# Optimization experiments

Measured on AMD Instinct MI355X. Metric: run time of the kernel, lower is better.

Reference implementation:

```python
import jax, jax.numpy as jnp
import numpy as np

B, NV, L, NKG = 8, 100, 128, 923
NT = NV + 1 + NKG  # 1024 total nodes
DV, DK, DH, H, NLAYERS, VOCAB = 2048, 300, 1024, 8, 3, 50265
DHD = DH // H


def _ln(x, g, b, eps=1e-5):
    m = x.mean(-1, keepdims=True)
    v = x.var(-1, keepdims=True)
    return (x - m) / jnp.sqrt(v + eps) * g + b


def _gat_layer(x, mask, W, bb, a_src, a_dst, ln_g, ln_b):
    # x: [B,N,D], mask: [B,N,N] bool
    Bn, N, D = x.shape
    h = (x @ W + bb).reshape(Bn, N, H, DHD)
    s = jnp.einsum('bnhd,hd->bnh', h, a_src)  # source term
    t = jnp.einsum('bnhd,hd->bnh', h, a_dst)  # target term
    e = jax.nn.leaky_relu(s[:, :, None, :] + t[:, None, :, :], 0.2)  # [B,N,N,H]
    e = jnp.where(mask[..., None], e, -1e9)
    a = jax.nn.softmax(e, axis=2)  # over neighbors j
    out = jnp.einsum('bijh,bjhd->bihd', a, h).reshape(Bn, N, D)
    return _ln(x + out, ln_g, ln_b)


def setup_inputs() -> dict:
    key = jax.random.key(0)
    ks = jax.random.split(key, 24)
    s = 0.02
    inp = {
        'visual_features': jax.random.normal(ks[0], (B, NV, DV), jnp.float32),
        'question_input_ids': jax.random.randint(ks[1], (B, L), 0, VOCAB, jnp.int64) if False else jax.random.randint(ks[1], (B, L), 0, VOCAB).astype(jnp.int32),
        'question_attention_mask': jnp.ones((B, L), jnp.int32),
        'graph_node_features': jax.random.normal(ks[2], (B, NKG, DK), jnp.float32),
        'graph_adj': jax.random.randint(ks[3], (B, NT, NT), 0, 2).astype(jnp.int32),
        'graph_node_types': jax.random.randint(ks[4], (B, NT), 0, 3).astype(jnp.int32),
        # params
        'vis_W': jax.random.normal(ks[5], (DV, DH), jnp.float32) * s,
        'vis_b': jnp.zeros((DH,), jnp.float32),
        'vis_ln_g': jnp.ones((DH,), jnp.float32),
        'vis_ln_b': jnp.zeros((DH,), jnp.float32),
        'tok_emb': jax.random.normal(ks[6], (VOCAB, DH), jnp.float32) * s,
        'q_W': jax.random.normal(ks[7], (DH, DH), jnp.float32) * s,
        'q_b': jnp.zeros((DH,), jnp.float32),
        'q_ln_g': jnp.ones((DH,), jnp.float32),
        'q_ln_b': jnp.zeros((DH,), jnp.float32),
        'kg_W': jax.random.normal(ks[8], (DK, DH), jnp.float32) * s,
        'kg_b': jnp.zeros((DH,), jnp.float32),
        'kg_ln_g': jnp.ones((DH,), jnp.float32),
        'kg_ln_b': jnp.zeros((DH,), jnp.float32),
        'type_emb': jax.random.normal(ks[9], (3, DH), jnp.float32) * s,
        'gat_W': jax.random.normal(ks[10], (NLAYERS, DH, DH), jnp.float32) * s,
        'gat_b': jnp.zeros((NLAYERS, DH), jnp.float32),
        'a_src': jax.random.normal(ks[11], (NLAYERS, H, DHD), jnp.float32) * s,
        'a_dst': jax.random.normal(ks[12], (NLAYERS, H, DHD), jnp.float32) * s,
        'gat_ln_g': jnp.ones((NLAYERS, DH), jnp.float32),
        'gat_ln_b': jnp.zeros((NLAYERS, DH), jnp.float32),
        'readout_W': jax.random.normal(ks[13], (DH, 1), jnp.float32) * s,
        'readout_b': jnp.zeros((1,), jnp.float32),
        'cs_W1': jax.random.normal(ks[14], (DH, DH), jnp.float32) * s,
        'cs_b1': jnp.zeros((DH,), jnp.float32),
        'cs_W2': jax.random.normal(ks[15], (DH, 1), jnp.float32) * s,
        'cs_b2': jnp.zeros((1,), jnp.float32),
    }
    return inp


def reference(visual_features, question_input_ids, question_attention_mask,
              graph_node_features, graph_adj, graph_node_types,
              vis_W, vis_b, vis_ln_g, vis_ln_b,
              tok_emb, q_W, q_b, q_ln_g, q_ln_b,
              kg_W, kg_b, kg_ln_g, kg_ln_b,
              type_emb, gat_W, gat_b, a_src, a_dst, gat_ln_g, gat_ln_b,
              readout_W, readout_b, cs_W1, cs_b1, cs_W2, cs_b2):
    # 1. visual projection
    vis = _ln(visual_features @ vis_W + vis_b, vis_ln_g, vis_ln_b)  # [B,NV,DH]
    # 2. text encoder (embedding + masked mean-pool + proj + LN)
    te = tok_emb[question_input_ids]  # [B,L,DH]
    m = question_attention_mask.astype(te.dtype)[..., None]
    pooled = (te * m).sum(1) / jnp.maximum(m.sum(1), 1.0)
    q = _ln(pooled @ q_W + q_b, q_ln_g, q_ln_b)[:, None, :]  # [B,1,DH]
    # 3. KG projection
    kg = _ln(graph_node_features @ kg_W + kg_b, kg_ln_g, kg_ln_b)
    # 4-5. concat + node-type embeddings
    x = jnp.concatenate([vis, q, kg], axis=1) + type_emb[graph_node_types]
    # 6. dense GAT stack
    mask = graph_adj > 0
    for l in range(NLAYERS):
        x = _gat_layer(x, mask, gat_W[l], gat_b[l], a_src[l], a_dst[l],
                       gat_ln_g[l], gat_ln_b[l])
    # 7. attention-pooled readout
    w = jax.nn.softmax((x @ readout_W + readout_b).squeeze(-1), axis=-1)
    g = (x * w[..., None]).sum(1)  # [B,DH]
    # 8. candidate scorer
    logits = jax.nn.gelu(g @ cs_W1 + cs_b1) @ cs_W2 + cs_b2  # [B,1]
    return logits
```

## Files before the change

### kernel.cpp

```cpp
#include <hip/hip_runtime.h>
#include <math.h>

#define NB 8
#define NV 100
#define LQ 128
#define NKG 923
#define NT 1024
#define DV 2048
#define DK 300
#define DH 1024
#define NH 8
#define DHD 128
#define NLAYERS 3

typedef __attribute__((ext_vector_type(8))) short short8;
typedef __attribute__((ext_vector_type(4))) float f32x4;

__device__ __forceinline__ short f2bf(float f) {
    unsigned u = __float_as_uint(f);
    u += 0x7fff + ((u >> 16) & 1);
    return (short)(u >> 16);
}
__device__ __forceinline__ float bf2f(short s) {
    unsigned u = ((unsigned)(unsigned short)s) << 16;
    return __uint_as_float(u);
}
__device__ __forceinline__ unsigned pack2(float a, float b) {
    return (unsigned)(unsigned short)f2bf(a) | ((unsigned)(unsigned short)f2bf(b) << 16);
}

#if __has_builtin(__builtin_amdgcn_global_load_lds)
#define HAVE_GLL 1
__device__ __forceinline__ void gll16(const void* g, void* l) {
    __builtin_amdgcn_global_load_lds(
        (const __attribute__((address_space(1))) void*)g,
        (__attribute__((address_space(3))) void*)l, 16, 0, 0);
}
#else
#define HAVE_GLL 0
#endif

__device__ __forceinline__ float block_reduce_sum(float v, float* red) {
    int tid = threadIdx.x;
    red[tid] = v; __syncthreads();
    for (int s = 128; s > 0; s >>= 1) {
        if (tid < s) red[tid] += red[tid + s];
        __syncthreads();
    }
    float r = red[0]; __syncthreads();
    return r;
}
__device__ __forceinline__ float block_reduce_max(float v, float* red) {
    int tid = threadIdx.x;
    red[tid] = v; __syncthreads();
    for (int s = 128; s > 0; s >>= 1) {
        if (tid < s) red[tid] = fmaxf(red[tid], red[tid + s]);
        __syncthreads();
    }
    float r = red[0]; __syncthreads();
    return r;
}

__global__ __launch_bounds__(256) void bitmask_kernel(
    const int* __restrict__ adj, unsigned* __restrict__ mb)
{
    int bi = blockIdx.x;
    int tid = threadIdx.x;
#pragma unroll
    for (int p = 0; p < 4; ++p) {
        int j = p * 256 + tid;
        unsigned long long bal = __ballot(adj[(size_t)bi * NT + j] > 0);
        if ((tid & 63) == 0) {
            int w = (p * 256 + (tid & 0xC0)) >> 5;
            mb[(size_t)bi * 32 + w]     = (unsigned)bal;
            mb[(size_t)bi * 32 + w + 1] = (unsigned)(bal >> 32);
        }
    }
}

__global__ __launch_bounds__(256) void transpose_cast(
    const float* __restrict__ in, short* __restrict__ out,
    int K, int N, int Kp)
{
    __shared__ float ls[64][65];
    int n0 = blockIdx.x * 64, k0 = blockIdx.y * 64;
    int tid = threadIdx.x;
    int j4 = (tid & 15) * 4;
#pragma unroll
    for (int s = 0; s < 4; ++s) {
        int i = (tid >> 4) + s * 16;
        int k = k0 + i;
        float4 v = make_float4(0.f, 0.f, 0.f, 0.f);
        if (k < K) v = *(const float4*)(in + (size_t)k * N + n0 + j4);
        ls[i][j4 + 0] = v.x; ls[i][j4 + 1] = v.y;
        ls[i][j4 + 2] = v.z; ls[i][j4 + 3] = v.w;
    }
    __syncthreads();
#pragma unroll
    for (int s = 0; s < 4; ++s) {
        int a = (tid >> 4) + s * 16;
        int b = (tid & 15) * 4;
        uint2 pk;
        pk.x = pack2(ls[b + 0][a], ls[b + 1][a]);
        pk.y = pack2(ls[b + 2][a], ls[b + 3][a]);
        *(uint2*)(out + (size_t)(n0 + a) * Kp + k0 + b) = pk;
    }
}

__global__ __launch_bounds__(256) void gemm_bias_mfma(
    const float* __restrict__ A, const short* __restrict__ Wt,
    const float* __restrict__ bias, float* __restrict__ C,
    int M, int N, int K, int Kp, int ldA)
{
    __shared__ short At[128][32];
    __shared__ short Bt[128][32];
    int tid = threadIdx.x;
    int row0 = blockIdx.y * 128, col0 = blockIdx.x * 128;
    int lane = tid & 63, wave = tid >> 6;
    int quad = lane >> 4, lq = lane & 15;
    int wm = (wave >> 1) * 64, wn = (wave & 1) * 64;
    f32x4 acc[4][4];
#pragma unroll
    for (int i = 0; i < 4; ++i)
#pragma unroll
        for (int j = 0; j < 4; ++j) {
            f32x4 z = {0.f, 0.f, 0.f, 0.f};
            acc[i][j] = z;
        }
    int ar = tid >> 2;
    int ac = (tid & 3) * 8;
    for (int k0 = 0; k0 < Kp; k0 += 32) {
        bool fullk = (k0 + 32 <= K);
#pragma unroll
        for (int s = 0; s < 2; ++s) {
            int r = ar + s * 64;
            int grow = row0 + r;
            short8 pk;
            if (grow < M && fullk) {
                const float* src = A + (size_t)grow * ldA + k0 + ac;
                float4 v0 = *(const float4*)(src);
                float4 v1 = *(const float4*)(src + 4);
                pk[0] = f2bf(v0.x); pk[1] = f2bf(v0.y);
                pk[2] = f2bf(v0.z); pk[3] = f2bf(v0.w);
                pk[4] = f2bf(v1.x); pk[5] = f2bf(v1.y);
                pk[6] = f2bf(v1.z); pk[7] = f2bf(v1.w);
            } else {
#pragma unroll
                for (int e = 0; e < 8; ++e) {
                    int k = k0 + ac + e;
                    pk[e] = (grow < M && k < K)
                          ? f2bf(A[(size_t)grow * ldA + k]) : (short)0;
                }
            }
            *(short8*)&At[r][ac] = pk;
        }
#pragma unroll
        for (int s = 0; s < 2; ++s) {
            int n = ar + s * 64;
            short8 w = *(const short8*)(Wt + (size_t)(col0 + n) * Kp + k0 + ac);
            *(short8*)&Bt[n][ac] = w;
        }
        __syncthreads();
        short8 af[4], bfr[4];
#pragma unroll
        for (int i = 0; i < 4; ++i)
            af[i] = *(short8*)&At[wm + i * 16 + lq][quad * 8];
#pragma unroll
        for (int j = 0; j < 4; ++j)
            bfr[j] = *(short8*)&Bt[wn + j * 16 + lq][quad * 8];
#pragma unroll
        for (int i = 0; i < 4; ++i)
#pragma unroll
            for (int j = 0; j < 4; ++j)
                acc[i][j] = __builtin_amdgcn_mfma_f32_16x16x32_bf16(
                    af[i], bfr[j], acc[i][j], 0, 0, 0);
        __syncthreads();
    }
#pragma unroll
    for (int j = 0; j < 4; ++j) {
        int n = col0 + wn + j * 16 + lq;
        float bv = bias[n];
#pragma unroll
        for (int i = 0; i < 4; ++i) {
#pragma unroll
            for (int r = 0; r < 4; ++r) {
                int m = row0 + wm + i * 16 + quad * 4 + r;
                if (m < M) C[(size_t)m * N + n] = acc[i][j][r] + bv;
            }
        }
    }
}

__global__ __launch_bounds__(256) void gemm_st_mfma(
    const short* __restrict__ Ab, const short* __restrict__ Wt,
    const float* __restrict__ bias,
    const float* __restrict__ asrc, const float* __restrict__ adst,
    short* __restrict__ ht,
    float* __restrict__ sbuf, float* __restrict__ tbuf)
{
    __shared__ __align__(16) short smem[17408];
    short (*At)[32]  = (short(*)[32])smem;
    short (*Bt)[32]  = (short(*)[32])(smem + 4096);
    short (*ct)[136] = (short(*)[136])smem;
    __shared__ float sred[2][128], tred[2][128];
    __shared__ float asl[128], adl[128];
    int tid = threadIdx.x;
    int h = blockIdx.x;
    int row0 = blockIdx.y * 128, col0 = h * 128;
    int b = row0 >> 10, i0 = row0 & 1023;
    int lane = tid & 63, wave = tid >> 6;
    int quad = lane >> 4, lq = lane & 15;
    int wm = (wave >> 1) * 64, wn = (wave & 1) * 64;
    if (tid < 128) asl[tid] = asrc[h * DHD + tid];
    else adl[tid - 128] = adst[h * DHD + tid - 128];
    f32x4 acc[4][4];
#pragma unroll
    for (int i = 0; i < 4; ++i)
#pragma unroll
        for (int j = 0; j < 4; ++j) {
            f32x4 z = {0.f, 0.f, 0.f, 0.f};
            acc[i][j] = z;
        }

    const short* gA0 = Ab + (size_t)(row0 + wave * 16 + (lane >> 2)) * DH + (lane & 3) * 8;
    const short* gA1 = gA0 + (size_t)64 * DH;
    const short* gB0 = Wt + (size_t)(col0 + wave * 16 + (lane >> 2)) * DH + (lane & 3) * 8;
    const short* gB1 = gB0 + (size_t)64 * DH;
#if HAVE_GLL
    char* lA0 = (char*)At + wave * 1024; char* lA1 = lA0 + 4096;
    char* lB0 = (char*)Bt + wave * 1024; char* lB1 = lB0 + 4096;
#endif
    for (int k0 = 0; k0 < DH; k0 += 32) {
#if HAVE_GLL
        gll16(gA0 + k0, lA0); gll16(gA1 + k0, lA1);
        gll16(gB0 + k0, lB0); gll16(gB1 + k0, lB1);
#else
        {
            short8 va0 = *(const short8*)(gA0 + k0);
            short8 va1 = *(const short8*)(gA1 + k0);
            short8 vb0 = *(const short8*)(gB0 + k0);
            short8 vb1 = *(const short8*)(gB1 + k0);
            *(short8*)((char*)At + wave * 1024 + lane * 16) = va0;
            *(short8*)((char*)At + 4096 + wave * 1024 + lane * 16) = va1;
            *(short8*)((char*)Bt + wave * 1024 + lane * 16) = vb0;
            *(short8*)((char*)Bt + 4096 + wave * 1024 + lane * 16) = vb1;
        }
#endif
        __syncthreads();
        short8 af[4], bfr[4];
#pragma unroll
        for (int i = 0; i < 4; ++i)
            af[i] = *(short8*)&At[wm + i * 16 + lq][quad * 8];
#pragma unroll
        for (int j = 0; j < 4; ++j)
            bfr[j] = *(short8*)&Bt[wn + j * 16 + lq][quad * 8];
#pragma unroll
        for (int i = 0; i < 4; ++i)
#pragma unroll
            for (int j = 0; j < 4; ++j)
                acc[i][j] = __builtin_amdgcn_mfma_f32_16x16x32_bf16(
                    af[i], bfr[j], acc[i][j], 0, 0, 0);
        __syncthreads();
    }
#pragma unroll
    for (int j = 0; j < 4; ++j) {
        int d = wn + j * 16 + lq;
        float bv = bias[col0 + d];
#pragma unroll
        for (int i2 = 0; i2 < 4; ++i2) {
            int m = wm + i2 * 16 + quad * 4;
            uint2 pk;
            pk.x = pack2(acc[i2][j][0] + bv, acc[i2][j][1] + bv);
            pk.y = pack2(acc[i2][j][2] + bv, acc[i2][j][3] + bv);
            *(uint2*)&ct[d][m] = pk;
        }
    }
    __syncthreads();
    {
        int d = tid >> 1, half = tid & 1;
        short* dst = ht + ((size_t)(b * NH + h) * DHD + d) * NT + i0 + half * 64;
        const short* src = &ct[d][half * 64];
#pragma unroll
        for (int q = 0; q < 8; ++q)
            *(short8*)(dst + q * 8) = *(const short8*)(src + q * 8);
    }
    {
        int i = tid >> 1, half = tid & 1;
        float sa = 0.f, ta = 0.f;
#pragma unroll 16
        for (int dd = 0; dd < 64; ++dd) {
            int d = half * 64 + dd;
            float hv = bf2f(ct[d][i]);
            sa += hv * asl[d];
            ta += hv * adl[d];
        }
        sred[half][i] = sa; tred[half][i] = ta;
    }
    __syncthreads();
    if (tid < 128) {
        size_t idx = (size_t)(b * NH + h) * NT + i0 + tid;
        sbuf[idx] = sred[0][tid] + sred[1][tid];
        tbuf[idx] = tred[0][tid] + tred[1][tid];
    }
}

__global__ __launch_bounds__(256) void ln_scatter(
    const float* __restrict__ src, float* __restrict__ x,
    const float* __restrict__ g, const float* __restrict__ bta,
    int rows, int npb, int node_off)
{
    __shared__ float red[256];
    int r = blockIdx.x;
    if (r >= rows) return;
    int tid = threadIdx.x;
    int b = r / npb, n = r % npb;
    float4 v = *(const float4*)(src + (size_t)r * DH + tid * 4);
    float s = v.x + v.y + v.z + v.w;
    float sq = v.x * v.x + v.y * v.y + v.z * v.z + v.w * v.w;
    float tot = block_reduce_sum(s, red);
    float totsq = block_reduce_sum(sq, red);
    float mean = tot * (1.0f / DH);
    float var = totsq * (1.0f / DH) - mean * mean;
    float rstd = 1.0f / sqrtf(var + 1e-5f);
    float4 gv = *(const float4*)(g + tid * 4);
    float4 bv = *(const float4*)(bta + tid * 4);
    float4 o;
    o.x = (v.x - mean) * rstd * gv.x + bv.x;
    o.y = (v.y - mean) * rstd * gv.y + bv.y;
    o.z = (v.z - mean) * rstd * gv.z + bv.z;
    o.w = (v.w - mean) * rstd * gv.w + bv.w;
    *(float4*)(x + ((size_t)(b * NT + node_off + n)) * DH + tid * 4) = o;
}

__global__ __launch_bounds__(256) void ln_residual(
    float* __restrict__ x, const float* __restrict__ o,
    const float* __restrict__ g, const float* __restrict__ bta,
    short* __restrict__ xb,
    const float* __restrict__ rW, const float* __restrict__ rb,
    float* __restrict__ scores)
{
    __shared__ float red[256];
    int r = blockIdx.x;
    int tid = threadIdx.x;
    float* xr = x + (size_t)r * DH;
    float4 xv = *(float4*)(xr + tid * 4);
    float4 ov = *(const float4*)(o + (size_t)r * DH + tid * 4);
    float v0 = xv.x + ov.x, v1 = xv.y + ov.y, v2 = xv.z + ov.z, v3 = xv.w + ov.w;
    float s = v0 + v1 + v2 + v3;
    float sq = v0 * v0 + v1 * v1 + v2 * v2 + v3 * v3;
    float tot = block_reduce_sum(s, red);
    float totsq = block_reduce_sum(sq, red);
    float mean = tot * (1.0f / DH);
    float var = totsq * (1.0f / DH) - mean * mean;
    float rstd = 1.0f / sqrtf(var + 1e-5f);
    float4 gv = *(const float4*)(g + tid * 4);
    float4 bv = *(const float4*)(bta + tid * 4);
    float4 out;
    out.x = (v0 - mean) * rstd * gv.x + bv.x;
    out.y = (v1 - mean) * rstd * gv.y + bv.y;
    out.z = (v2 - mean) * rstd * gv.z + bv.z;
    out.w = (v3 - mean) * rstd * gv.w + bv.w;
    *(float4*)(xr + tid * 4) = out;
    uint2 pk;
    pk.x = pack2(out.x, out.y);
    pk.y = pack2(out.z, out.w);
    *(uint2*)(xb + (size_t)r * DH + tid * 4) = pk;
    if (scores) {
        float4 wv = *(const float4*)(rW + tid * 4);
        float p = out.x * wv.x + out.y * wv.y + out.z * wv.z + out.w * wv.w;
        float totp = block_reduce_sum(p, red);
        if (tid == 0) scores[r] = totp + rb[0];
    }
}

__global__ __launch_bounds__(256) void pool_kernel(
    const float* __restrict__ tok_emb, const int* __restrict__ ids,
    const int* __restrict__ amask, float* __restrict__ pooled)
{
    int b = blockIdx.x;
    int tid = threadIdx.x;
    float a0 = 0, a1 = 0, a2 = 0, a3 = 0;
    float denom = 0;
    for (int l = 0; l < LQ; ++l) {
        int id = ids[b * LQ + l];
        float m = (float)amask[b * LQ + l];
        denom += m;
        float4 e = *(const float4*)(tok_emb + (size_t)id * DH + tid * 4);
        a0 += m * e.x; a1 += m * e.y; a2 += m * e.z; a3 += m * e.w;
    }
    float inv = 1.0f / fmaxf(denom, 1.0f);
    float4 o = make_float4(a0 * inv, a1 * inv, a2 * inv, a3 * inv);
    *(float4*)(pooled + b * DH + tid * 4) = o;
}

__global__ __launch_bounds__(256) void type_add(
    float* __restrict__ x, const int* __restrict__ types,
    const float* __restrict__ type_emb, short* __restrict__ xb)
{
    int r = blockIdx.x;
    int tid = threadIdx.x;
    int ty = types[r];
    float4 xv = *(float4*)(x + (size_t)r * DH + tid * 4);
    float4 tv = *(const float4*)(type_emb + (size_t)ty * DH + tid * 4);
    xv.x += tv.x; xv.y += tv.y; xv.z += tv.z; xv.w += tv.w;
    *(float4*)(x + (size_t)r * DH + tid * 4) = xv;
    uint2 pk;
    pk.x = pack2(xv.x, xv.y);
    pk.y = pack2(xv.z, xv.w);
    *(uint2*)(xb + (size_t)r * DH + tid * 4) = pk;
}

__global__ __launch_bounds__(256) void agg_mfma(
    const short* __restrict__ ht, const unsigned* __restrict__ mb,
    const float* __restrict__ s, const float* __restrict__ t,
    float* __restrict__ obuf)
{
    __shared__ short vt[128][72];
    __shared__ short at[64][72];
    __shared__ unsigned mrow[64][32];
    __shared__ float sv[64], alpha_s[64], lfin[64];
    int i0 = blockIdx.x * 64;
    int h = blockIdx.y, b = blockIdx.z;
    int tid = threadIdx.x;
    int lane = tid & 63, wave = tid >> 6;
    int quad = lane >> 4, lq = lane & 15;
    int wi = (wave >> 1) * 32;
    int wd = (wave & 1) * 64;
    if (tid < 64) sv[tid] = s[(size_t)(b * NH + h) * NT + i0 + tid];
#pragma unroll
    for (int s2 = 0; s2 < 2; ++s2) {
        int f = tid + s2 * 256;
        int ii2 = f >> 3, w4 = (f & 7) * 4;
        *(uint4*)&mrow[ii2][w4] =
            *(const uint4*)(mb + ((size_t)(b * NT + i0 + ii2)) * 32 + w4);
    }
    const float* tptr = t + (size_t)(b * NH + h) * NT;
    const short* hbase = ht + ((size_t)(b * NH + h) * DHD) * NT;
    f32x4 acc[2][4];
#pragma unroll
    for (int i = 0; i < 2; ++i)
#pragma unroll
        for (int j = 0; j < 4; ++j) {
            f32x4 z = {0.f, 0.f, 0.f, 0.f};
            acc[i][j] = z;
        }
    int ii = tid >> 2;
    int jq = (tid & 3) * 16;
    float m_run = -3e38f, l_run = 0.f;
    for (int j0 = 0; j0 < NT; j0 += 64) {
        __syncthreads();
#pragma unroll
        for (int s2 = 0; s2 < 4; ++s2) {
            int f = tid + s2 * 256;
            int d = f >> 3, c = (f & 7) * 8;
            *(short8*)&vt[d][c] = *(const short8*)(hbase + (size_t)d * NT + j0 + c);
        }
        float vv[16];
        unsigned mw;
        float tmax = -3e38f;
        {
            mw = mrow[ii][(j0 + jq) >> 5] >> ((j0 + jq) & 31);
            float svv = sv[ii];
            float4 t0 = *(const float4*)(tptr + j0 + jq);
            float4 t1 = *(const float4*)(tptr + j0 + jq + 4);
            float4 t2 = *(const float4*)(tptr + j0 + jq + 8);
            float4 t3 = *(const float4*)(tptr + j0 + jq + 12);
            float tv16[16] = {t0.x, t0.y, t0.z, t0.w, t1.x, t1.y, t1.z, t1.w,
                              t2.x, t2.y, t2.z, t2.w, t3.x, t3.y, t3.z, t3.w};
#pragma unroll
            for (int e = 0; e < 16; ++e) {
                float v = svv + tv16[e];
                v = v > 0.f ? v : 0.2f * v;
                v = ((mw >> e) & 1) ? v : -1e9f;
                vv[e] = v;
                tmax = fmaxf(tmax, v);
            }
        }
        tmax = fmaxf(tmax, __shfl_xor(tmax, 1, 64));
        tmax = fmaxf(tmax, __shfl_xor(tmax, 2, 64));
        float m_new = fmaxf(m_run, tmax);
        float al = __expf(m_run - m_new);
        float tsum = 0.f;
        short8 p0, p1;
#pragma unroll
        for (int e = 0; e < 8; ++e) {
            float w = ((mw >> e) & 1) ? __expf(vv[e] - m_new) : 0.f;
            tsum += w; p0[e] = f2bf(w);
        }
#pragma unroll
        for (int e = 0; e < 8; ++e) {
            float w = ((mw >> (8 + e)) & 1) ? __expf(vv[8 + e] - m_new) : 0.f;
            tsum += w; p1[e] = f2bf(w);
        }
        tsum += __shfl_xor(tsum, 1, 64);
        tsum += __shfl_xor(tsum, 2, 64);
        l_run = l_run * al + tsum;
        m_run = m_new;
        *(short8*)&at[ii][jq] = p0;
        *(short8*)&at[ii][jq + 8] = p1;
        if ((tid & 3) == 0) alpha_s[ii] = al;
        __syncthreads();
#pragma unroll
        for (int i2 = 0; i2 < 2; ++i2)
#pragma unroll
            for (int r = 0; r < 4; ++r) {
                float arow = alpha_s[wi + i2 * 16 + quad * 4 + r];
#pragma unroll
                for (int j = 0; j < 4; ++j) acc[i2][j][r] *= arow;
            }
#pragma unroll
        for (int ks = 0; ks < 2; ++ks) {
            short8 af[2], bfr[4];
            af[0] = *(short8*)&at[wi + lq][ks * 32 + quad * 8];
            af[1] = *(short8*)&at[wi + 16 + lq][ks * 32 + quad * 8];
#pragma unroll
            for (int j = 0; j < 4; ++j)
                bfr[j] = *(short8*)&vt[wd + j * 16 + lq][ks * 32 + quad * 8];
#pragma unroll
            for (int i2 = 0; i2 < 2; ++i2)
#pragma unroll
                for (int j = 0; j < 4; ++j)
                    acc[i2][j] = __builtin_amdgcn_mfma_f32_16x16x32_bf16(
                        af[i2], bfr[j], acc[i2][j], 0, 0, 0);
        }
    }
    if ((tid & 3) == 0) lfin[ii] = l_run;
    __syncthreads();
#pragma unroll
    for (int i2 = 0; i2 < 2; ++i2) {
#pragma unroll
        for (int r = 0; r < 4; ++r) {
            int il = wi + i2 * 16 + quad * 4 + r;
            float inv = 1.0f / lfin[il];
            float* dst = obuf + ((size_t)(b * NT + i0 + il)) * DH + h * DHD + wd;
#pragma unroll
            for (int j = 0; j < 4; ++j)
                dst[j * 16 + lq] = acc[i2][j][r] * inv;
        }
    }
}

__global__ __launch_bounds__(256) void pool_part(
    const float* __restrict__ x, const float* __restrict__ scores,
    float* __restrict__ gpart)
{
    __shared__ float red[256];
    int p = blockIdx.x;
    int b = blockIdx.y;
    int tid = threadIdx.x;
    const float* sr = scores + (size_t)b * NT;
    float v[4];
    float mx = -3e38f;
#pragma unroll
    for (int k = 0; k < 4; ++k) { v[k] = sr[tid + k * 256]; mx = fmaxf(mx, v[k]); }
    float m = block_reduce_max(mx, red);
    float ls = 0.f;
#pragma unroll
    for (int k = 0; k < 4; ++k) ls += expf(v[k] - m);
    float tot = block_reduce_sum(ls, red);
    float inv = 1.0f / tot;
    float a0 = 0, a1 = 0, a2 = 0, a3 = 0;
    for (int n = p * 128; n < (p + 1) * 128; ++n) {
        float wv = expf(sr[n] - m) * inv;
        float4 xv = *(const float4*)(x + ((size_t)(b * NT + n)) * DH + tid * 4);
        a0 += wv * xv.x; a1 += wv * xv.y; a2 += wv * xv.z; a3 += wv * xv.w;
    }
    float4 o = make_float4(a0, a1, a2, a3);
    *(float4*)(gpart + ((size_t)(b * 8 + p)) * DH + tid * 4) = o;
}

__global__ __launch_bounds__(256) void scorer_kernel(
    const float* __restrict__ gpart, const float* __restrict__ W1,
    const float* __restrict__ b1, const float* __restrict__ W2,
    const float* __restrict__ b2, float* __restrict__ out)
{
    __shared__ float gsh[DH];
    __shared__ float red[256];
    int b = blockIdx.x;
    int tid = threadIdx.x;
#pragma unroll
    for (int c = 0; c < 4; ++c) {
        int d = tid + c * 256;
        float gv = 0.f;
        for (int p = 0; p < 8; ++p) gv += gpart[((size_t)(b * 8 + p)) * DH + d];
        gsh[d] = gv;
    }
    __syncthreads();
    float acc[4] = {};
    for (int d = 0; d < DH; ++d) {
        float gv = gsh[d];
        const float* wr = W1 + (size_t)d * DH;
#pragma unroll
        for (int c = 0; c < 4; ++c) acc[c] += gv * wr[tid + c * 256];
    }
    float part = 0.f;
#pragma unroll
    for (int c = 0; c < 4; ++c) {
        int k = tid + c * 256;
        float u = acc[c] + b1[k];
        float inner = 0.7978845608028654f * (u + 0.044715f * u * u * u);
        float gel = 0.5f * u * (1.0f + tanhf(inner));
        part += gel * W2[k];
    }
    float tot = block_reduce_sum(part, red);
    if (tid == 0) out[b] = tot + b2[0];
}

extern "C" void kernel_launch(void* const* d_in, const int* in_sizes, int n_in,
                              void* d_out, int out_size, void* d_ws, size_t ws_size,
                              hipStream_t stream)
{
    const float* visual   = (const float*)d_in[0];
    const int*   q_ids    = (const int*)d_in[1];
    const int*   q_mask   = (const int*)d_in[2];
    const float* kg_feat  = (const float*)d_in[3];
    const int*   adj      = (const int*)d_in[4];
    const int*   ntypes   = (const int*)d_in[5];
    const float* vis_W    = (const float*)d_in[6];
    const float* vis_b    = (const float*)d_in[7];
    const float* vis_lng  = (const float*)d_in[8];
    const float* vis_lnb  = (const float*)d_in[9];
    const float* tok_emb  = (const float*)d_in[10];
    const float* q_W      = (const float*)d_in[11];
    const float* q_b      = (const float*)d_in[12];
    const float* q_lng    = (const float*)d_in[13];
    const float* q_lnb    = (const float*)d_in[14];
    const float* kg_W     = (const float*)d_in[15];
    const float* kg_b     = (const float*)d_in[16];
    const float* kg_lng   = (const float*)d_in[17];
    const float* kg_lnb   = (const float*)d_in[18];
    const float* type_emb = (const float*)d_in[19];
    const float* gat_W    = (const float*)d_in[20];
    const float* gat_b    = (const float*)d_in[21];
    const float* a_src    = (const float*)d_in[22];
    const float* a_dst    = (const float*)d_in[23];
    const float* gat_lng  = (const float*)d_in[24];
    const float* gat_lnb  = (const float*)d_in[25];
    const float* read_W   = (const float*)d_in[26];
    const float* read_b   = (const float*)d_in[27];
    const float* cs_W1    = (const float*)d_in[28];
    const float* cs_b1    = (const float*)d_in[29];
    const float* cs_W2    = (const float*)d_in[30];
    const float* cs_b2    = (const float*)d_in[31];
    float* out = (float*)d_out;

    float* ws = (float*)d_ws;
    const size_t NROW = (size_t)NB * NT;
    float* x      = ws;
    float* obuf   = x + NROW * DH;
    float* sbuf   = obuf + NROW * DH;
    float* tbuf   = sbuf + NB * NH * NT;
    float* pooled = tbuf + NB * NH * NT;
    float* scores = pooled + NB * DH;
    float* gpart  = scores + NROW;
    short* wt_gat = (short*)(gpart + NB * 8 * DH);
    short* ht     = wt_gat + (size_t)NLAYERS * DH * DH;
    unsigned* mb  = (unsigned*)(ht + (size_t)NB * NH * DHD * NT);
    short* xb     = (short*)(mb + (size_t)NB * NT * 32);
    short* wt_vis = xb + NROW * DH;
    short* wt_q   = wt_vis + (size_t)1024 * 2048;
    short* wt_kg  = wt_q + (size_t)1024 * 1024;

    transpose_cast<<<dim3(16, 32), 256, 0, stream>>>(vis_W, wt_vis, DV, DH, DV);
    transpose_cast<<<dim3(16, 16), 256, 0, stream>>>(q_W, wt_q, DH, DH, DH);
    transpose_cast<<<dim3(16, 5), 256, 0, stream>>>(kg_W, wt_kg, DK, DH, 320);
    for (int l = 0; l < NLAYERS; ++l)
        transpose_cast<<<dim3(16, 16), 256, 0, stream>>>(
            gat_W + (size_t)l * DH * DH, wt_gat + (size_t)l * DH * DH, DH, DH, DH);
    bitmask_kernel<<<NB * NT, 256, 0, stream>>>(adj, mb);

    gemm_bias_mfma<<<dim3(8, 7), 256, 0, stream>>>(
        visual, wt_vis, vis_b, obuf, NB * NV, DH, DV, DV, DV);
    ln_scatter<<<NB * NV, 256, 0, stream>>>(obuf, x, vis_lng, vis_lnb, NB * NV, NV, 0);

    pool_kernel<<<NB, 256, 0, stream>>>(tok_emb, q_ids, q_mask, pooled);
    gemm_bias_mfma<<<dim3(8, 1), 256, 0, stream>>>(
        pooled, wt_q, q_b, obuf, NB, DH, DH, DH, DH);
    ln_scatter<<<NB, 256, 0, stream>>>(obuf, x, q_lng, q_lnb, NB, 1, NV);

    gemm_bias_mfma<<<dim3(8, 58), 256, 0, stream>>>(
        kg_feat, wt_kg, kg_b, obuf, NB * NKG, DH, DK, 320, DK);
    ln_scatter<<<NB * NKG, 256, 0, stream>>>(obuf, x, kg_lng, kg_lnb, NB * NKG, NKG, NV + 1);

    type_add<<<NB * NT, 256, 0, stream>>>(x, ntypes, type_emb, xb);

    for (int l = 0; l < NLAYERS; ++l) {
        const float* bl  = gat_b + (size_t)l * DH;
        const float* asl = a_src + (size_t)l * NH * DHD;
        const float* adl = a_dst + (size_t)l * NH * DHD;
        gemm_st_mfma<<<dim3(NH, 64), 256, 0, stream>>>(
            xb, wt_gat + (size_t)l * DH * DH, bl, asl, adl, ht, sbuf, tbuf);
        agg_mfma<<<dim3(16, NH, NB), 256, 0, stream>>>(
            ht, mb, sbuf, tbuf, obuf);
        ln_residual<<<NB * NT, 256, 0, stream>>>(x, obuf,
            gat_lng + (size_t)l * DH, gat_lnb + (size_t)l * DH, xb,
            read_W, read_b, (l == NLAYERS - 1) ? scores : nullptr);
    }

    pool_part<<<dim3(8, NB), 256, 0, stream>>>(x, scores, gpart);
    scorer_kernel<<<NB, 256, 0, stream>>>(gpart, cs_W1, cs_b1, cs_W2, cs_b2, out);
}
```

Baseline: 1.057 ms.

## Fuse type embedding into LN, use wave-shuffle reductions, split pooling and scorer, swizzle agg LDS

```diff
diff --git a/kernel.cpp b/kernel.cpp
--- a/kernel.cpp
+++ b/kernel.cpp
@@ -40,24 +40,34 @@
 #define HAVE_GLL 0
 #endif
 
-__device__ __forceinline__ float block_reduce_sum(float v, float* red) {
-    int tid = threadIdx.x;
-    red[tid] = v; __syncthreads();
-    for (int s = 128; s > 0; s >>= 1) {
-        if (tid < s) red[tid] += red[tid + s];
-        __syncthreads();
-    }
-    float r = red[0]; __syncthreads();
-    return r;
-}
-__device__ __forceinline__ float block_reduce_max(float v, float* red) {
-    int tid = threadIdx.x;
-    red[tid] = v; __syncthreads();
-    for (int s = 128; s > 0; s >>= 1) {
-        if (tid < s) red[tid] = fmaxf(red[tid], red[tid + s]);
-        __syncthreads();
-    }
-    float r = red[0]; __syncthreads();
+__device__ __forceinline__ float block_sum1(float a, float* red4) {
+#pragma unroll
+    for (int off = 32; off > 0; off >>= 1) a += __shfl_xor(a, off, 64);
+    int w = threadIdx.x >> 6;
+    if ((threadIdx.x & 63) == 0) red4[w] = a;
+    __syncthreads();
+    return red4[0] + red4[1] + red4[2] + red4[3];
+}
+__device__ __forceinline__ float block_max1(float a, float* red4) {
+#pragma unroll
+    for (int off = 32; off > 0; off >>= 1) a = fmaxf(a, __shfl_xor(a, off, 64));
+    int w = threadIdx.x >> 6;
+    if ((threadIdx.x & 63) == 0) red4[w] = a;
+    __syncthreads();
+    return fmaxf(fmaxf(red4[0], red4[1]), fmaxf(red4[2], red4[3]));
+}
+__device__ __forceinline__ float2 block_sum2(float a, float b, float* red8) {
+#pragma unroll
+    for (int off = 32; off > 0; off >>= 1) {
+        a += __shfl_xor(a, off, 64);
+        b += __shfl_xor(b, off, 64);
+    }
+    int w = threadIdx.x >> 6;
+    if ((threadIdx.x & 63) == 0) { red8[w] = a; red8[4 + w] = b; }
+    __syncthreads();
+    float2 r;
+    r.x = red8[0] + red8[1] + red8[2] + red8[3];
+    r.y = red8[4] + red8[5] + red8[6] + red8[7];
     return r;
 }
 
@@ -80,9 +90,11 @@
 
 __global__ __launch_bounds__(256) void transpose_cast(
     const float* __restrict__ in, short* __restrict__ out,
-    int K, int N, int Kp)
+    int K, int N, int Kp, size_t in_stride, size_t out_stride)
 {
     __shared__ float ls[64][65];
+    const float* inL = in + (size_t)blockIdx.z * in_stride;
+    short* outL = out + (size_t)blockIdx.z * out_stride;
     int n0 = blockIdx.x * 64, k0 = blockIdx.y * 64;
     int tid = threadIdx.x;
     int j4 = (tid & 15) * 4;
@@ -91,7 +103,7 @@
         int i = (tid >> 4) + s * 16;
         int k = k0 + i;
         float4 v = make_float4(0.f, 0.f, 0.f, 0.f);
-        if (k < K) v = *(const float4*)(in + (size_t)k * N + n0 + j4);
+        if (k < K) v = *(const float4*)(inL + (size_t)k * N + n0 + j4);
         ls[i][j4 + 0] = v.x; ls[i][j4 + 1] = v.y;
         ls[i][j4 + 2] = v.z; ls[i][j4 + 3] = v.w;
     }
@@ -103,7 +115,7 @@
         uint2 pk;
         pk.x = pack2(ls[b + 0][a], ls[b + 1][a]);
         pk.y = pack2(ls[b + 2][a], ls[b + 3][a]);
-        *(uint2*)(out + (size_t)(n0 + a) * Kp + k0 + b) = pk;
+        *(uint2*)(outL + (size_t)(n0 + a) * Kp + k0 + b) = pk;
     }
 }
 
@@ -307,29 +319,37 @@
 __global__ __launch_bounds__(256) void ln_scatter(
     const float* __restrict__ src, float* __restrict__ x,
     const float* __restrict__ g, const float* __restrict__ bta,
+    const int* __restrict__ types, const float* __restrict__ type_emb,
+    short* __restrict__ xb,
     int rows, int npb, int node_off)
 {
-    __shared__ float red[256];
+    __shared__ float red[8];
     int r = blockIdx.x;
     if (r >= rows) return;
     int tid = threadIdx.x;
-    int b = r / npb, n = r % npb;
+    int b = r / npb, n = r - b * npb;
+    int node = b * NT + node_off + n;
     float4 v = *(const float4*)(src + (size_t)r * DH + tid * 4);
     float s = v.x + v.y + v.z + v.w;
     float sq = v.x * v.x + v.y * v.y + v.z * v.z + v.w * v.w;
-    float tot = block_reduce_sum(s, red);
-    float totsq = block_reduce_sum(sq, red);
-    float mean = tot * (1.0f / DH);
-    float var = totsq * (1.0f / DH) - mean * mean;
+    float2 t2 = block_sum2(s, sq, red);
+    float mean = t2.x * (1.0f / DH);
+    float var = t2.y * (1.0f / DH) - mean * mean;
     float rstd = 1.0f / sqrtf(var + 1e-5f);
     float4 gv = *(const float4*)(g + tid * 4);
     float4 bv = *(const float4*)(bta + tid * 4);
+    int ty = types[node];
+    float4 tv = *(const float4*)(type_emb + (size_t)ty * DH + tid * 4);
     float4 o;
-    o.x = (v.x - mean) * rstd * gv.x + bv.x;
-    o.y = (v.y - mean) * rstd * gv.y + bv.y;
-    o.z = (v.z - mean) * rstd * gv.z + bv.z;
-    o.w = (v.w - mean) * rstd * gv.w + bv.w;
-    *(float4*)(x + ((size_t)(b * NT + node_off + n)) * DH + tid * 4) = o;
+    o.x = (v.x - mean) * rstd * gv.x + bv.x + tv.x;
+    o.y = (v.y - mean) * rstd * gv.y + bv.y + tv.y;
+    o.z = (v.z - mean) * rstd * gv.z + bv.z + tv.z;
+    o.w = (v.w - mean) * rstd * gv.w + bv.w + tv.w;
+    *(float4*)(x + (size_t)node * DH + tid * 4) = o;
+    uint2 pk;
+    pk.x = pack2(o.x, o.y);
+    pk.y = pack2(o.z, o.w);
+    *(uint2*)(xb + (size_t)node * DH + tid * 4) = pk;
 }
 
 __global__ __launch_bounds__(256) void ln_residual(
@@ -339,7 +359,7 @@
     const float* __restrict__ rW, const float* __restrict__ rb,
     float* __restrict__ scores)
 {
-    __shared__ float red[256];
+    __shared__ float red[12];
     int r = blockIdx.x;
     int tid = threadIdx.x;
     float* xr = x + (size_t)r * DH;
@@ -348,10 +368,9 @@
     float v0 = xv.x + ov.x, v1 = xv.y + ov.y, v2 = xv.z + ov.z, v3 = xv.w + ov.w;
     float s = v0 + v1 + v2 + v3;
     float sq = v0 * v0 + v1 * v1 + v2 * v2 + v3 * v3;
-    float tot = block_reduce_sum(s, red);
-    float totsq = block_reduce_sum(sq, red);
-    float mean = tot * (1.0f / DH);
-    float var = totsq * (1.0f / DH) - mean * mean;
+    float2 t2 = block_sum2(s, sq, red);
+    float mean = t2.x * (1.0f / DH);
+    float var = t2.y * (1.0f / DH) - mean * mean;
     float rstd = 1.0f / sqrtf(var + 1e-5f);
     float4 gv = *(const float4*)(g + tid * 4);
     float4 bv = *(const float4*)(bta + tid * 4);
@@ -368,46 +387,47 @@
     if (scores) {
         float4 wv = *(const float4*)(rW + tid * 4);
         float p = out.x * wv.x + out.y * wv.y + out.z * wv.z + out.w * wv.w;
-        float totp = block_reduce_sum(p, red);
+        float totp = block_sum1(p, red + 8);
         if (tid == 0) scores[r] = totp + rb[0];
     }
 }
 
-__global__ __launch_bounds__(256) void pool_kernel(
+__global__ __launch_bounds__(256) void qpool_part(
     const float* __restrict__ tok_emb, const int* __restrict__ ids,
-    const int* __restrict__ amask, float* __restrict__ pooled)
-{
-    int b = blockIdx.x;
+    const int* __restrict__ amask, float* __restrict__ ppool,
+    float* __restrict__ pden)
+{
+    int b = blockIdx.x, c = blockIdx.y;
     int tid = threadIdx.x;
     float a0 = 0, a1 = 0, a2 = 0, a3 = 0;
     float denom = 0;
-    for (int l = 0; l < LQ; ++l) {
+    for (int l = c * 32; l < (c + 1) * 32; ++l) {
         int id = ids[b * LQ + l];
         float m = (float)amask[b * LQ + l];
         denom += m;
         float4 e = *(const float4*)(tok_emb + (size_t)id * DH + tid * 4);
         a0 += m * e.x; a1 += m * e.y; a2 += m * e.z; a3 += m * e.w;
     }
-    float inv = 1.0f / fmaxf(denom, 1.0f);
-    float4 o = make_float4(a0 * inv, a1 * inv, a2 * inv, a3 * inv);
+    float4 o = make_float4(a0, a1, a2, a3);
+    *(float4*)(ppool + ((size_t)(b * 4 + c)) * DH + tid * 4) = o;
+    if (tid == 0) pden[b * 4 + c] = denom;
+}
+__global__ __launch_bounds__(256) void qpool_fin(
+    const float* __restrict__ ppool, const float* __restrict__ pden,
+    float* __restrict__ pooled)
+{
+    int b = blockIdx.x;
+    int tid = threadIdx.x;
+    float den = pden[b * 4] + pden[b * 4 + 1] + pden[b * 4 + 2] + pden[b * 4 + 3];
+    float inv = 1.0f / fmaxf(den, 1.0f);
+    float4 s = make_float4(0.f, 0.f, 0.f, 0.f);
+#pragma unroll
+    for (int c = 0; c < 4; ++c) {
+        float4 v = *(const float4*)(ppool + ((size_t)(b * 4 + c)) * DH + tid * 4);
+        s.x += v.x; s.y += v.y; s.z += v.z; s.w += v.w;
+    }
+    float4 o = make_float4(s.x * inv, s.y * inv, s.z * inv, s.w * inv);
     *(float4*)(pooled + b * DH + tid * 4) = o;
-}
-
-__global__ __launch_bounds__(256) void type_add(
-    float* __restrict__ x, const int* __restrict__ types,
-    const float* __restrict__ type_emb, short* __restrict__ xb)
-{
-    int r = blockIdx.x;
-    int tid = threadIdx.x;
-    int ty = types[r];
-    float4 xv = *(float4*)(x + (size_t)r * DH + tid * 4);
-    float4 tv = *(const float4*)(type_emb + (size_t)ty * DH + tid * 4);
-    xv.x += tv.x; xv.y += tv.y; xv.z += tv.z; xv.w += tv.w;
-    *(float4*)(x + (size_t)r * DH + tid * 4) = xv;
-    uint2 pk;
-    pk.x = pack2(xv.x, xv.y);
-    pk.y = pack2(xv.z, xv.w);
-    *(uint2*)(xb + (size_t)r * DH + tid * 4) = pk;
 }
 
 __global__ __launch_bounds__(256) void agg_mfma(
@@ -415,7 +435,7 @@
     const float* __restrict__ s, const float* __restrict__ t,
     float* __restrict__ obuf)
 {
-    __shared__ short vt[128][72];
+    __shared__ __align__(16) short vt[128 * 64];
     __shared__ short at[64][72];
     __shared__ unsigned mrow[64][32];
     __shared__ float sv[64], alpha_s[64], lfin[64];
@@ -436,6 +456,15 @@
     }
     const float* tptr = t + (size_t)(b * NH + h) * NT;
     const short* hbase = ht + ((size_t)(b * NH + h) * DHD) * NT;
+    const short* gsrc[4];
+    char* ldst[4];
+#pragma unroll
+    for (int s2 = 0; s2 < 4; ++s2) {
+        int f = tid + s2 * 256;
+        int d = f >> 3, cc = f & 7;
+        gsrc[s2] = hbase + (size_t)d * NT + ((cc ^ (d & 7)) * 8);
+        ldst[s2] = (char*)vt + wave * 1024 + s2 * 4096;
+    }
     f32x4 acc[2][4];
 #pragma unroll
     for (int i = 0; i < 2; ++i)
@@ -449,12 +478,17 @@
     float m_run = -3e38f, l_run = 0.f;
     for (int j0 = 0; j0 < NT; j0 += 64) {
         __syncthreads();
+#if HAVE_GLL
+#pragma unroll
+        for (int s2 = 0; s2 < 4; ++s2) gll16(gsrc[s2] + j0, ldst[s2]);
+#else
 #pragma unroll
         for (int s2 = 0; s2 < 4; ++s2) {
             int f = tid + s2 * 256;
-            int d = f >> 3, c = (f & 7) * 8;
-            *(short8*)&vt[d][c] = *(const short8*)(hbase + (size_t)d * NT + j0 + c);
-        }
+            short8 v8 = *(const short8*)(gsrc[s2] + j0);
+            *(short8*)((char*)vt + (size_t)f * 16) = v8;
+        }
+#endif
         float vv[16];
         unsigned mw;
         float tmax = -3e38f;
@@ -508,14 +542,17 @@
 #pragma unroll
                 for (int j = 0; j < 4; ++j) acc[i2][j][r] *= arow;
             }
+        const char* vtb = (const char*)vt;
 #pragma unroll
         for (int ks = 0; ks < 2; ++ks) {
             short8 af[2], bfr[4];
             af[0] = *(short8*)&at[wi + lq][ks * 32 + quad * 8];
             af[1] = *(short8*)&at[wi + 16 + lq][ks * 32 + quad * 8];
+            int cc = ks * 4 + quad;
+            int sx = (cc ^ (lq & 7)) * 16;
 #pragma unroll
             for (int j = 0; j < 4; ++j)
-                bfr[j] = *(short8*)&vt[wd + j * 16 + lq][ks * 32 + quad * 8];
+                bfr[j] = *(const short8*)(vtb + (wd + j * 16 + lq) * 128 + sx);
 #pragma unroll
             for (int i2 = 0; i2 < 2; ++i2)
 #pragma unroll
@@ -544,7 +581,7 @@
     const float* __restrict__ x, const float* __restrict__ scores,
     float* __restrict__ gpart)
 {
-    __shared__ float red[256];
+    __shared__ float red[8];
     int p = blockIdx.x;
     int b = blockIdx.y;
     int tid = threadIdx.x;
@@ -553,11 +590,11 @@
     float mx = -3e38f;
 #pragma unroll
     for (int k = 0; k < 4; ++k) { v[k] = sr[tid + k * 256]; mx = fmaxf(mx, v[k]); }
-    float m = block_reduce_max(mx, red);
+    float m = block_max1(mx, red);
     float ls = 0.f;
 #pragma unroll
     for (int k = 0; k < 4; ++k) ls += expf(v[k] - m);
-    float tot = block_reduce_sum(ls, red);
+    float tot = block_sum1(ls, red + 4);
     float inv = 1.0f / tot;
     float a0 = 0, a1 = 0, a2 = 0, a3 = 0;
     for (int n = p * 128; n < (p + 1) * 128; ++n) {
@@ -569,40 +606,53 @@
     *(float4*)(gpart + ((size_t)(b * 8 + p)) * DH + tid * 4) = o;
 }
 
-__global__ __launch_bounds__(256) void scorer_kernel(
+__global__ __launch_bounds__(256) void scorer_part(
     const float* __restrict__ gpart, const float* __restrict__ W1,
-    const float* __restrict__ b1, const float* __restrict__ W2,
-    const float* __restrict__ b2, float* __restrict__ out)
-{
-    __shared__ float gsh[DH];
-    __shared__ float red[256];
-    int b = blockIdx.x;
-    int tid = threadIdx.x;
-#pragma unroll
-    for (int c = 0; c < 4; ++c) {
-        int d = tid + c * 256;
+    float* __restrict__ spart)
+{
+    __shared__ float gsh[128];
+    int c = blockIdx.x, b = blockIdx.y;
+    int tid = threadIdx.x;
+    if (tid < 128) {
+        int d = c * 128 + tid;
         float gv = 0.f;
+#pragma unroll
         for (int p = 0; p < 8; ++p) gv += gpart[((size_t)(b * 8 + p)) * DH + d];
-        gsh[d] = gv;
+        gsh[tid] = gv;
     }
     __syncthreads();
     float acc[4] = {};
-    for (int d = 0; d < DH; ++d) {
-        float gv = gsh[d];
-        const float* wr = W1 + (size_t)d * DH;
-#pragma unroll
-        for (int c = 0; c < 4; ++c) acc[c] += gv * wr[tid + c * 256];
-    }
+    for (int dd = 0; dd < 128; ++dd) {
+        float gv = gsh[dd];
+        const float* wr = W1 + (size_t)(c * 128 + dd) * DH;
+#pragma unroll
+        for (int cc = 0; cc < 4; ++cc) acc[cc] += gv * wr[tid + cc * 256];
+    }
+#pragma unroll
+    for (int cc = 0; cc < 4; ++cc)
+        spart[((size_t)(b * 8 + c)) * DH + tid + cc * 256] = acc[cc];
+}
+__global__ __launch_bounds__(256) void scorer_fin(
+    const float* __restrict__ spart, const float* __restrict__ b1,
+    const float* __restrict__ W2, const float* __restrict__ b2,
+    float* __restrict__ out)
+{
+    __shared__ float red[4];
+    int b = blockIdx.x;
+    int tid = threadIdx.x;
     float part = 0.f;
 #pragma unroll
-    for (int c = 0; c < 4; ++c) {
-        int k = tid + c * 256;
-        float u = acc[c] + b1[k];
+    for (int cc = 0; cc < 4; ++cc) {
+        int k = tid + cc * 256;
+        float s = 0.f;
+#pragma unroll
+        for (int c = 0; c < 8; ++c) s += spart[((size_t)(b * 8 + c)) * DH + k];
+        float u = s + b1[k];
         float inner = 0.7978845608028654f * (u + 0.044715f * u * u * u);
         float gel = 0.5f * u * (1.0f + tanhf(inner));
         part += gel * W2[k];
     }
-    float tot = block_reduce_sum(part, red);
+    float tot = block_sum1(part, red);
     if (tid == 0) out[b] = tot + b2[0];
 }
 
@@ -653,7 +703,10 @@
     float* pooled = tbuf + NB * NH * NT;
     float* scores = pooled + NB * DH;
     float* gpart  = scores + NROW;
-    short* wt_gat = (short*)(gpart + NB * 8 * DH);
+    float* ppool  = gpart + NB * 8 * DH;
+    float* pden   = ppool + NB * 4 * DH;
+    float* spart  = pden + 64;
+    short* wt_gat = (short*)(spart + NB * 8 * DH);
     short* ht     = wt_gat + (size_t)NLAYERS * DH * DH;
     unsigned* mb  = (unsigned*)(ht + (size_t)NB * NH * DHD * NT);
     short* xb     = (short*)(mb + (size_t)NB * NT * 32);
@@ -661,28 +714,29 @@
     short* wt_q   = wt_vis + (size_t)1024 * 2048;
     short* wt_kg  = wt_q + (size_t)1024 * 1024;
 
-    transpose_cast<<<dim3(16, 32), 256, 0, stream>>>(vis_W, wt_vis, DV, DH, DV);
-    transpose_cast<<<dim3(16, 16), 256, 0, stream>>>(q_W, wt_q, DH, DH, DH);
-    transpose_cast<<<dim3(16, 5), 256, 0, stream>>>(kg_W, wt_kg, DK, DH, 320);
-    for (int l = 0; l < NLAYERS; ++l)
-        transpose_cast<<<dim3(16, 16), 256, 0, stream>>>(
-            gat_W + (size_t)l * DH * DH, wt_gat + (size_t)l * DH * DH, DH, DH, DH);
+    transpose_cast<<<dim3(16, 32, 1), 256, 0, stream>>>(vis_W, wt_vis, DV, DH, DV, 0, 0);
+    transpose_cast<<<dim3(16, 16, 1), 256, 0, stream>>>(q_W, wt_q, DH, DH, DH, 0, 0);
+    transpose_cast<<<dim3(16, 5, 1), 256, 0, stream>>>(kg_W, wt_kg, DK, DH, 320, 0, 0);
+    transpose_cast<<<dim3(16, 16, NLAYERS), 256, 0, stream>>>(
+        gat_W, wt_gat, DH, DH, DH, (size_t)DH * DH, (size_t)DH * DH);
     bitmask_kernel<<<NB * NT, 256, 0, stream>>>(adj, mb);
 
     gemm_bias_mfma<<<dim3(8, 7), 256, 0, stream>>>(
         visual, wt_vis, vis_b, obuf, NB * NV, DH, DV, DV, DV);
-    ln_scatter<<<NB * NV, 256, 0, stream>>>(obuf, x, vis_lng, vis_lnb, NB * NV, NV, 0);
-
-    pool_kernel<<<NB, 256, 0, stream>>>(tok_emb, q_ids, q_mask, pooled);
+    ln_scatter<<<NB * NV, 256, 0, stream>>>(obuf, x, vis_lng, vis_lnb,
+        ntypes, type_emb, xb, NB * NV, NV, 0);
+
+    qpool_part<<<dim3(NB, 4), 256, 0, stream>>>(tok_emb, q_ids, q_mask, ppool, pden);
+    qpool_fin<<<NB, 256, 0, stream>>>(ppool, pden, pooled);
     gemm_bias_mfma<<<dim3(8, 1), 256, 0, stream>>>(
         pooled, wt_q, q_b, obuf, NB, DH, DH, DH, DH);
-    ln_scatter<<<NB, 256, 0, stream>>>(obuf, x, q_lng, q_lnb, NB, 1, NV);
+    ln_scatter<<<NB, 256, 0, stream>>>(obuf, x, q_lng, q_lnb,
+        ntypes, type_emb, xb, NB, 1, NV);
 
     gemm_bias_mfma<<<dim3(8, 58), 256, 0, stream>>>(
         kg_feat, wt_kg, kg_b, obuf, NB * NKG, DH, DK, 320, DK);
-    ln_scatter<<<NB * NKG, 256, 0, stream>>>(obuf, x, kg_lng, kg_lnb, NB * NKG, NKG, NV + 1);
-
-    type_add<<<NB * NT, 256, 0, stream>>>(x, ntypes, type_emb, xb);
+    ln_scatter<<<NB * NKG, 256, 0, stream>>>(obuf, x, kg_lng, kg_lnb,
+        ntypes, type_emb, xb, NB * NKG, NKG, NV + 1);
 
     for (int l = 0; l < NLAYERS; ++l) {
         const float* bl  = gat_b + (size_t)l * DH;
@@ -698,5 +752,6 @@
     }
 
     pool_part<<<dim3(8, NB), 256, 0, stream>>>(x, scores, gpart);
-    scorer_kernel<<<NB, 256, 0, stream>>>(gpart, cs_W1, cs_b1, cs_W2, cs_b2, out);
-}
+    scorer_part<<<dim3(8, NB), 256, 0, stream>>>(gpart, cs_W1, spart);
+    scorer_fin<<<NB, 256, 0, stream>>>(spart, cs_b1, cs_W2, cs_b2, out);
+}
```

Measured after the change: 948.5 us. -10.3%, faster.
